# Optimization experiments

Hardware: AMD Instinct MI355X
Metric: run time of the kernel (lower is better)

The kernel has to match this reference:

```python
import jax, jax.numpy as jnp
import numpy as np

VOC_SHAPE = (100, 100, 100)   # m_k factors of voc_size = 1_000_000
EMB_SHAPE = (4, 4, 8)         # n_k factors of emb_size = 128
RANK = 16
PAD_IDX = 0
VOC = int(np.prod(VOC_SHAPE))
EMB = int(np.prod(EMB_SHAPE))


def setup_inputs() -> dict:
    key = jax.random.key(0)
    k0, k1, k2, kx = jax.random.split(key, 4)
    # TT-matrix cores [r_k, m_k, n_k, r_{k+1}], boundary ranks = 1.
    # Per-core std chosen so the reconstructed table has stddev near
    # target_stddev = sqrt(2/voc_size) (the 'nn' init intent); exact init
    # distribution is irrelevant to the math being tested.
    d = 3
    target_std = np.sqrt(2.0 / VOC)
    core_std = float((target_std / RANK ** ((d - 1) / 2.0)) ** (1.0 / d))
    core0 = jax.random.normal(k0, (1, VOC_SHAPE[0], EMB_SHAPE[0], RANK), jnp.float32) * core_std
    core1 = jax.random.normal(k1, (RANK, VOC_SHAPE[1], EMB_SHAPE[1], RANK), jnp.float32) * core_std
    core2 = jax.random.normal(k2, (RANK, VOC_SHAPE[2], EMB_SHAPE[2], 1), jnp.float32) * core_std
    x = jax.random.randint(kx, (64, 512), 0, VOC, dtype=jnp.int64)
    return {"x": x, "core0": core0, "core1": core1, "core2": core2}


def _tt_full(core0, core1, core2):
    # Sequential TT-matrix contraction, as in sample_full():
    # res accumulates shape (m1*n1*...*mk*nk, r_{k+1})
    res = core0.reshape(-1, core0.shape[-1])                      # (m1*n1, r1)
    res = res @ core1.reshape(core1.shape[0], -1)                 # (m1*n1, m2*n2*r2)
    res = res.reshape(-1, core2.shape[0]) @ core2.reshape(core2.shape[0], -1)
    # (m1, n1, m2, n2, m3, n3) -> (m1, m2, m3, n1, n2, n3) -> (VOC, EMB)
    m1, m2, m3 = VOC_SHAPE
    n1, n2, n3 = EMB_SHAPE
    full = res.reshape(m1, n1, m2, n2, m3, n3)
    full = full.transpose(0, 2, 4, 1, 3, 5).reshape(VOC, EMB)
    return full


def reference(x, core0, core1, core2):
    xshape = x.shape
    x_flat = x.reshape(-1)
    full = _tt_full(core0, core1, core2)          # [VOC, EMB] materialized table
    rows = full[x_flat]                           # gather [B*S, EMB]
    rows = jnp.where(x_flat[:, None] != PAD_IDX, rows, jnp.zeros_like(rows))
    return rows.reshape(*xshape, EMB)
```

## Files before the change

kernel.cpp:

```cpp
#include <hip/hip_runtime.h>
#include <hip/hip_bf16.h>


#define LDS_PER_WAVE 704

__global__ __launch_bounds__(256) void tt_embed_kernel(
    const int* __restrict__ x,
    const float* __restrict__ c0,
    const float* __restrict__ c1,
    const float* __restrict__ c2,
    float* __restrict__ out,
    int nTok)
{
    __shared__ float lds[4 * LDS_PER_WAVE];
    const int wave = threadIdx.x >> 6;
    const int lane = threadIdx.x & 63;
    const int t = blockIdx.x * 4 + wave;
    const bool active = (t < nTok);

    float* As = lds + wave * LDS_PER_WAVE;
    float* Cs = As + 64;
    float* Ms = Cs + 128;

    int idx = 0;
    if (active) idx = x[t];
    const int i1 = idx / 10000;
    const int rem = idx - i1 * 10000;
    const int i2 = rem / 100;
    const int i3 = rem - i2 * 100;

    if (active) {
        if (lane < 16) {
            ((float4*)As)[lane] = *(const float4*)(c0 + i1 * 64 + lane * 4);
        } else if (lane < 48) {
            const int l = lane - 16;
            const int r2 = l >> 1;
            const int half = l & 1;
            ((float4*)Cs)[l] = *(const float4*)(c2 + (r2 * 100 + i3) * 8 + half * 4);
        }
    }

    const int r1 = lane >> 2;
    const int j2 = lane & 3;
    float bb[16];
    if (active) {
        const float4* bp = (const float4*)(c1 + ((r1 * 100 + i2) * 4 + j2) * 16);
        float4 b0 = bp[0], b1 = bp[1], b2 = bp[2], b3 = bp[3];
        bb[0]=b0.x; bb[1]=b0.y; bb[2]=b0.z; bb[3]=b0.w;
        bb[4]=b1.x; bb[5]=b1.y; bb[6]=b1.z; bb[7]=b1.w;
        bb[8]=b2.x; bb[9]=b2.y; bb[10]=b2.z; bb[11]=b2.w;
        bb[12]=b3.x; bb[13]=b3.y; bb[14]=b3.z; bb[15]=b3.w;
    } else {
        #pragma unroll
        for (int j = 0; j < 16; ++j) bb[j] = 0.0f;
    }

    __syncthreads();

    float mv[8];
    #pragma unroll
    for (int j = 0; j < 8; ++j) mv[j] = 0.0f;
    #pragma unroll
    for (int r2 = 0; r2 < 16; ++r2) {
        const float4* cp = (const float4*)(Cs + r2 * 8);
        float4 ca = cp[0];
        float4 cb = cp[1];
        const float b = bb[r2];
        mv[0] += b * ca.x; mv[1] += b * ca.y; mv[2] += b * ca.z; mv[3] += b * ca.w;
        mv[4] += b * cb.x; mv[5] += b * cb.y; mv[6] += b * cb.z; mv[7] += b * cb.w;
    }
    {
        float4* mp = (float4*)(Ms + lane * 8);
        mp[0] = make_float4(mv[0], mv[1], mv[2], mv[3]);
        mp[1] = make_float4(mv[4], mv[5], mv[6], mv[7]);
    }

    __syncthreads();

    const int e0 = lane * 2;
    const int j1 = e0 >> 5;
    const int mcol = e0 & 31;

    const float4* ap = (const float4*)(As + j1 * 16);
    float4 a0 = ap[0], a1 = ap[1], a2 = ap[2], a3 = ap[3];
    float av[16] = { a0.x, a0.y, a0.z, a0.w, a1.x, a1.y, a1.z, a1.w,
                     a2.x, a2.y, a2.z, a2.w, a3.x, a3.y, a3.z, a3.w };

    float o0 = 0.0f, o1 = 0.0f;
    #pragma unroll
    for (int r = 0; r < 16; ++r) {
        const float2 m = *(const float2*)(Ms + r * 32 + mcol);
        o0 += av[r] * m.x;
        o1 += av[r] * m.y;
    }

    if (idx == 0) { o0 = 0.0f; o1 = 0.0f; }

    if (active) {
        *(float2*)(out + (long)t * 128 + e0) = make_float2(o0, o1);
    }
}

extern "C" void kernel_launch(void* const* d_in, const int* in_sizes, int n_in,
                              void* d_out, int out_size, void* d_ws, size_t ws_size,
                              hipStream_t stream) {
    const int*   x  = (const int*)d_in[0];
    const float* c0 = (const float*)d_in[1];
    const float* c1 = (const float*)d_in[2];
    const float* c2 = (const float*)d_in[3];
    float* out = (float*)d_out;

    const int nTok = out_size / 128;
    const int blocks = (nTok + 3) / 4;
    tt_embed_kernel<<<dim3(blocks), dim3(256), 0, stream>>>(x, c0, c1, c2, out, nTok);
}
```

Measured before the change: 80.33 us.

## Reorder TT contraction to contract core0 with core1 first via LDS staging

Changes the contraction order so that core0 (transposed into LDS) is first combined with core1, whose slice is loaded cooperatively into LDS with coalesced float4 loads. The intermediate is written to a padded LDS buffer (stride 17) and then contracted with core2. This replaces per-lane strided register loads of core1 with coalesced cooperative loads. In exchange it uses roughly twice the LDS per wave and has scalar, possibly bank-conflicting LDS reads.

Result: no change. 81.89 us (+1.9%).

```diff
diff --git a/kernel.cpp b/kernel.cpp
--- a/kernel.cpp
+++ b/kernel.cpp
@@ -2,7 +2,11 @@
 #include <hip/hip_bf16.h>
 
 
-#define LDS_PER_WAVE 704
+#define AT_OFF 0
+#define CS_OFF 64
+#define BS_OFF 192
+#define TS_OFF 1216
+#define LDS_PER_WAVE 1488
 
 __global__ __launch_bounds__(256) void tt_embed_kernel(
     const int* __restrict__ x,
@@ -18,9 +22,10 @@
     const int t = blockIdx.x * 4 + wave;
     const bool active = (t < nTok);
 
-    float* As = lds + wave * LDS_PER_WAVE;
-    float* Cs = As + 64;
-    float* Ms = Cs + 128;
+    float* At = lds + wave * LDS_PER_WAVE + AT_OFF;
+    float* Cs = lds + wave * LDS_PER_WAVE + CS_OFF;
+    float* Bs = lds + wave * LDS_PER_WAVE + BS_OFF;
+    float* Ts = lds + wave * LDS_PER_WAVE + TS_OFF;
 
     int idx = 0;
     if (active) idx = x[t];
@@ -30,74 +35,61 @@
     const int i3 = rem - i2 * 100;
 
     if (active) {
-        if (lane < 16) {
-            ((float4*)As)[lane] = *(const float4*)(c0 + i1 * 64 + lane * 4);
-        } else if (lane < 48) {
-            const int l = lane - 16;
-            const int r2 = l >> 1;
-            const int half = l & 1;
-            ((float4*)Cs)[l] = *(const float4*)(c2 + (r2 * 100 + i3) * 8 + half * 4);
+        {
+            const int j1 = lane >> 4;
+            const int r1 = lane & 15;
+            At[r1 * 4 + j1] = c0[i1 * 64 + j1 * 16 + r1];
         }
-    }
-
-    const int r1 = lane >> 2;
-    const int j2 = lane & 3;
-    float bb[16];
-    if (active) {
-        const float4* bp = (const float4*)(c1 + ((r1 * 100 + i2) * 4 + j2) * 16);
-        float4 b0 = bp[0], b1 = bp[1], b2 = bp[2], b3 = bp[3];
-        bb[0]=b0.x; bb[1]=b0.y; bb[2]=b0.z; bb[3]=b0.w;
-        bb[4]=b1.x; bb[5]=b1.y; bb[6]=b1.z; bb[7]=b1.w;
-        bb[8]=b2.x; bb[9]=b2.y; bb[10]=b2.z; bb[11]=b2.w;
-        bb[12]=b3.x; bb[13]=b3.y; bb[14]=b3.z; bb[15]=b3.w;
-    } else {
+        if (lane < 32) {
+            const int r2 = lane >> 1;
+            const int half = lane & 1;
+            ((float4*)Cs)[lane] = *(const float4*)(c2 + (r2 * 100 + i3) * 8 + half * 4);
+        }
         #pragma unroll
-        for (int j = 0; j < 16; ++j) bb[j] = 0.0f;
+        for (int k = 0; k < 4; ++k) {
+            const int f = k * 64 + lane;
+            const int r1 = f >> 4;
+            const int w = f & 15;
+            ((float4*)Bs)[f] = *((const float4*)(c1 + (r1 * 100 + i2) * 64) + w);
+        }
     }
 
     __syncthreads();
 
-    float mv[8];
+    const int j2 = lane & 3;
+    const int r2s = lane >> 2;
+    float tac[4] = {0.f, 0.f, 0.f, 0.f};
     #pragma unroll
-    for (int j = 0; j < 8; ++j) mv[j] = 0.0f;
+    for (int r1 = 0; r1 < 16; ++r1) {
+        const float4 a4 = *(const float4*)(At + r1 * 4);
+        const float b = Bs[r1 * 64 + j2 * 16 + r2s];
+        tac[0] += a4.x * b;
+        tac[1] += a4.y * b;
+        tac[2] += a4.z * b;
+        tac[3] += a4.w * b;
+    }
     #pragma unroll
-    for (int r2 = 0; r2 < 16; ++r2) {
-        const float4* cp = (const float4*)(Cs + r2 * 8);
-        float4 ca = cp[0];
-        float4 cb = cp[1];
-        const float b = bb[r2];
-        mv[0] += b * ca.x; mv[1] += b * ca.y; mv[2] += b * ca.z; mv[3] += b * ca.w;
-        mv[4] += b * cb.x; mv[5] += b * cb.y; mv[6] += b * cb.z; mv[7] += b * cb.w;
-    }
-    {
-        float4* mp = (float4*)(Ms + lane * 8);
-        mp[0] = make_float4(mv[0], mv[1], mv[2], mv[3]);
-        mp[1] = make_float4(mv[4], mv[5], mv[6], mv[7]);
+    for (int j1 = 0; j1 < 4; ++j1) {
+        Ts[(j1 * 4 + j2) * 17 + r2s] = tac[j1];
     }
 
     __syncthreads();
 
-    const int e0 = lane * 2;
-    const int j1 = e0 >> 5;
-    const int mcol = e0 & 31;
-
-    const float4* ap = (const float4*)(As + j1 * 16);
-    float4 a0 = ap[0], a1 = ap[1], a2 = ap[2], a3 = ap[3];
-    float av[16] = { a0.x, a0.y, a0.z, a0.w, a1.x, a1.y, a1.z, a1.w,
-                     a2.x, a2.y, a2.z, a2.w, a3.x, a3.y, a3.z, a3.w };
-
-    float o0 = 0.0f, o1 = 0.0f;
+    const int q = lane >> 2;
+    const int j3 = (2 * lane) & 7;
+    float o0 = 0.f, o1 = 0.f;
     #pragma unroll
-    for (int r = 0; r < 16; ++r) {
-        const float2 m = *(const float2*)(Ms + r * 32 + mcol);
-        o0 += av[r] * m.x;
-        o1 += av[r] * m.y;
+    for (int r2 = 0; r2 < 16; ++r2) {
+        const float tv = Ts[q * 17 + r2];
+        const float2 cv = *(const float2*)(Cs + r2 * 8 + j3);
+        o0 += tv * cv.x;
+        o1 += tv * cv.y;
     }
 
-    if (idx == 0) { o0 = 0.0f; o1 = 0.0f; }
+    if (idx == 0) { o0 = 0.f; o1 = 0.f; }
 
     if (active) {
-        *(float2*)(out + (long)t * 128 + e0) = make_float2(o0, o1);
+        *(float2*)(out + (long)t * 128 + 2 * lane) = make_float2(o0, o1);
     }
 }
 
```
